# Kernel tuning notes

Measured on AMD Instinct MI355X. Metric: run time of the kernel, lower is better.

Reference implementation:

```python
import jax, jax.numpy as jnp
import numpy as np

N, E, F_IN, H, G, C = 50000, 800000, 128, 4, 32, 4
NEG_SLOPE = 0.2
EPS_GN = 1e-5


def setup_inputs() -> dict:
    key = jax.random.key(0)
    ks = iter(jax.random.split(key, 64))
    def gl(shape, fan):
        return jax.random.normal(next(ks), shape, jnp.float32) / np.float32(np.sqrt(fan))
    inp = {}
    inp['x'] = jax.random.normal(next(ks), (N, F_IN), jnp.float32)
    inp['edge_index'] = jax.random.randint(next(ks), (2, E), 0, N, dtype=jnp.int32)
    inp['batch'] = jnp.sort(jax.random.randint(next(ks), (N,), 0, G, dtype=jnp.int32))
    inp['Wl1'] = gl((F_IN, H * 64), F_IN); inp['bl1'] = jnp.zeros((H * 64,), jnp.float32)
    inp['Wr1'] = gl((F_IN, H * 64), F_IN); inp['br1'] = jnp.zeros((H * 64,), jnp.float32)
    inp['att1'] = gl((H, 64), 64); inp['bias1'] = jnp.zeros((H * 64,), jnp.float32)
    inp['gw1'] = jnp.ones((H * 64,), jnp.float32); inp['gb1'] = jnp.zeros((H * 64,), jnp.float32); inp['ga1'] = jnp.ones((H * 64,), jnp.float32)
    inp['Wl2'] = gl((256, H * 32), 256); inp['bl2'] = jnp.zeros((H * 32,), jnp.float32)
    inp['Wr2'] = gl((256, H * 32), 256); inp['br2'] = jnp.zeros((H * 32,), jnp.float32)
    inp['att2'] = gl((H, 32), 32); inp['bias2'] = jnp.zeros((H * 32,), jnp.float32)
    inp['gw2'] = jnp.ones((H * 32,), jnp.float32); inp['gb2'] = jnp.zeros((H * 32,), jnp.float32); inp['ga2'] = jnp.ones((H * 32,), jnp.float32)
    # GATv2 layer 3: 128 -> 16, 4 heads averaged (concat=False)
    inp['Wl3'] = gl((128, H * 16), 128); inp['bl3'] = jnp.zeros((H * 16,), jnp.float32)
    inp['Wr3'] = gl((128, H * 16), 128); inp['br3'] = jnp.zeros((H * 16,), jnp.float32)
    inp['att3'] = gl((H, 16), 16); inp['bias3'] = jnp.zeros((16,), jnp.float32)
    inp['gw3'] = jnp.ones((16,), jnp.float32); inp['gb3'] = jnp.zeros((16,), jnp.float32); inp['ga3'] = jnp.ones((16,), jnp.float32)
    # final linear 16 -> C
    inp['linW'] = gl((16, C), 16); inp['linB'] = jnp.zeros((C,), jnp.float32)
    return inp


def _gatv2(x, src, dst, Wl, bl, Wr, br, att, bias, D, concat):
    n = x.shape[0]
    xl = (x @ Wl + bl).reshape(n, H, D)   # source-side transform
    xr = (x @ Wr + br).reshape(n, H, D)   # target-side transform
    m = xl[src] + xr[dst]                  # [E', H, D]
    s = jnp.einsum('ehd,hd->eh', jax.nn.leaky_relu(m, NEG_SLOPE), att)
    smax = jax.ops.segment_max(s, dst, num_segments=n)
    e = jnp.exp(s - smax[dst])
    denom = jax.ops.segment_sum(e, dst, num_segments=n)
    alpha = e / (denom[dst] + 1e-16)       # softmax over incoming edges
    out = jax.ops.segment_sum(alpha[:, :, None] * xl[src], dst, num_segments=n)
    out = out.reshape(n, H * D) if concat else out.mean(axis=1)
    return out + bias


def _graphnorm(x, batch, w, b, a):
    cnt = jnp.maximum(jax.ops.segment_sum(jnp.ones((x.shape[0],), x.dtype), batch, num_segments=G), 1.0)
    mean = jax.ops.segment_sum(x, batch, num_segments=G) / cnt[:, None]
    xc = x - a * mean[batch]
    var = jax.ops.segment_sum(xc * xc, batch, num_segments=G) / cnt[:, None]
    return w * xc / jnp.sqrt(var[batch] + EPS_GN) + b


def reference(x, edge_index, batch,
              Wl1, bl1, Wr1, br1, att1, bias1, gw1, gb1, ga1,
              Wl2, bl2, Wr2, br2, att2, bias2, gw2, gb2, ga2,
              Wl3, bl3, Wr3, br3, att3, bias3, gw3, gb3, ga3,
              linW, linB):
    n = x.shape[0]
    ar = jnp.arange(n, dtype=edge_index.dtype)
    src = jnp.concatenate([edge_index[0], ar])  # add self-loops (PyG default)
    dst = jnp.concatenate([edge_index[1], ar])
    h = jax.nn.relu(_graphnorm(_gatv2(x, src, dst, Wl1, bl1, Wr1, br1, att1, bias1, 64, True), batch, gw1, gb1, ga1))
    h = jax.nn.relu(_graphnorm(_gatv2(h, src, dst, Wl2, bl2, Wr2, br2, att2, bias2, 32, True), batch, gw2, gb2, ga2))
    h = jax.nn.relu(_graphnorm(_gatv2(h, src, dst, Wl3, bl3, Wr3, br3, att3, bias3, 16, False), batch, gw3, gb3, ga3))
    cnt = jnp.maximum(jax.ops.segment_sum(jnp.ones((n,), h.dtype), batch, num_segments=G), 1.0)
    features = jax.ops.segment_sum(h, batch, num_segments=G) / cnt[:, None]  # global mean pool [G,16]
    logits = features @ linW + linB
    return (logits, features)
```

## Files before the change

kernel.cpp:

```cpp
#include <hip/hip_runtime.h>
#include <cstdint>


#define NEG_SLOPE 0.2f

typedef __attribute__((ext_vector_type(8))) short short8;
typedef __attribute__((ext_vector_type(4))) float f32x4;
typedef _Float16 h2 __attribute__((ext_vector_type(2)));
union U16 { uint4 u; short8 s; };

__device__ inline unsigned short f2bf_rne(float x) {
  unsigned u = __float_as_uint(x);
  return (unsigned short)((u + 0x7fff + ((u >> 16) & 1)) >> 16);
}
__device__ inline unsigned short f2h_bits(float x) {
  _Float16 h = (_Float16)x;
  return __builtin_bit_cast(unsigned short, h);
}
__device__ inline float h2f(unsigned short h) {
  return (float)__builtin_bit_cast(_Float16, h);
}
__device__ inline h2 u2h2(unsigned u) { return __builtin_bit_cast(h2, u); }

__device__ inline float fdot2h(h2 a, h2 b, float c) {
#if __has_builtin(__builtin_amdgcn_fdot2)
  return __builtin_amdgcn_fdot2(a, b, c, false);
#else
  return c + (float)a.x * (float)b.x + (float)a.y * (float)b.y;
#endif
}

__device__ inline int wave_incl_scan(int v, int lane) {
#pragma unroll
  for (int ofs = 1; ofs < 64; ofs <<= 1) {
    int t = __shfl_up(v, ofs, 64);
    if (lane >= ofs) v += t;
  }
  return v;
}

__global__ void deg_batch_hist(const int* __restrict__ ei, const int* __restrict__ batch,
                               int* __restrict__ deg, int* __restrict__ cnt, int E, int N) {
  __shared__ int h[32];
  if (threadIdx.x < 32) h[threadIdx.x] = 0;
  __syncthreads();
  int i = blockIdx.x * blockDim.x + threadIdx.x;
  int ET = E + N;
  if (i < ET) {
    int d = (i < E) ? ei[E + i] : (i - E);
    atomicAdd(&deg[d], 1);
  }
  if (i < N) atomicAdd(&h[batch[i]], 1);
  __syncthreads();
  if (threadIdx.x < 32 && h[threadIdx.x] > 0) atomicAdd(&cnt[threadIdx.x], h[threadIdx.x]);
}

__global__ void chunk_sums(const int* __restrict__ deg, int* __restrict__ bsum, int n) {
  int tid = threadIdx.x, lane = tid & 63, wid = tid >> 6;
  int i = blockIdx.x * 1024 + tid;
  int v = (i < n) ? deg[i] : 0;
#pragma unroll
  for (int m = 32; m; m >>= 1) v += __shfl_xor(v, m, 64);
  __shared__ int ws[16];
  if (lane == 0) ws[wid] = v;
  __syncthreads();
  if (tid == 0) {
    int s = 0;
    for (int k = 0; k < 16; ++k) s += ws[k];
    bsum[blockIdx.x] = s;
  }
}

__global__ void scan_apply(const int* __restrict__ deg, const int* __restrict__ bsum,
                           int* __restrict__ off, int nb, int n) {
  __shared__ int ws[16];
  __shared__ int sb[64];
  int tid = threadIdx.x, lane = tid & 63, wid = tid >> 6;
  if (wid == 0) {
    int v = (lane < nb) ? bsum[lane] : 0;
    int incl = wave_incl_scan(v, lane);
    sb[lane] = incl;
  }
  __syncthreads();
  int boff = (blockIdx.x > 0) ? sb[blockIdx.x - 1] : 0;
  if (blockIdx.x == 0 && tid == 0) off[n] = sb[nb - 1];
  int i = blockIdx.x * 1024 + tid;
  int v = (i < n) ? deg[i] : 0;
  int incl = wave_incl_scan(v, lane);
  if (lane == 63) ws[wid] = incl;
  __syncthreads();
  if (wid == 0) {
    int t = (lane < 16) ? ws[lane] : 0;
    t = wave_incl_scan(t, lane);
    if (lane < 16) ws[lane] = t;
  }
  __syncthreads();
  int wpre = (wid > 0) ? ws[wid - 1] : 0;
  if (i < n) off[i] = boff + wpre + incl - v;
}

__global__ void scatter_edges(const int* __restrict__ ei, const int* __restrict__ off,
                              int* __restrict__ cur, int* __restrict__ csr_src,
                              int E, int N) {
  int i = blockIdx.x * blockDim.x + threadIdx.x;
  int ET = E + N;
  if (i >= ET) return;
  int s, d;
  if (i < E) { s = ei[i]; d = ei[E + i]; } else { s = d = i - E; }
  int pos = off[d] + atomicAdd(&cur[d], 1);
  csr_src[pos] = s;
}

__device__ inline void wprep_body(const float* __restrict__ W, unsigned short* __restrict__ pk,
                                  int K, int M, int t) {
  int nk = K >> 5;
  int total = (M >> 4) * nk * 512;
  if (t >= total) return;
  int j = t & 7;
  int l = (t >> 3) & 63;
  int rest = t >> 9;
  int kc = rest % nk;
  int ct = rest / nk;
  int k = (kc << 5) + ((l >> 4) << 3) + j;
  int col = (ct << 4) + (l & 15);
  float w = W[(size_t)k * M + col];
  unsigned u = __float_as_uint(w);
  unsigned short hi = (unsigned short)(u >> 16);
  float hif = __uint_as_float(u & 0xffff0000u);
  unsigned short lo = f2bf_rne(w - hif);
  unsigned short* dst = pk + ((size_t)(ct * nk + kc) * 64 + l) * 16;
  dst[j] = hi;
  dst[j + 8] = lo;
}

__global__ void wprep_all(const float* W0, const float* W1, const float* W2,
                          const float* W3, const float* W4, const float* W5,
                          unsigned short* p0, unsigned short* p1, unsigned short* p2,
                          unsigned short* p3, unsigned short* p4, unsigned short* p5) {
  int t = blockIdx.x * 256 + threadIdx.x;
  switch (blockIdx.y) {
    case 0: wprep_body(W0, p0, 128, 256, t); break;
    case 1: wprep_body(W1, p1, 128, 256, t); break;
    case 2: wprep_body(W2, p2, 256, 128, t); break;
    case 3: wprep_body(W3, p3, 256, 128, t); break;
    case 4: wprep_body(W4, p4, 128, 64, t); break;
    default: wprep_body(W5, p5, 128, 64, t); break;
  }
}

__device__ inline void gemm_epilogue(
    unsigned short* __restrict__ sb0, unsigned short* __restrict__ sb1,
    f32x4* accL, f32x4* accR,
    const float* __restrict__ biasL, const float* __restrict__ biasR,
    unsigned short* __restrict__ CL, unsigned short* __restrict__ CR,
    int N, int M, int c0g, int row0blk) {
  int wv = threadIdx.x >> 6, lane = threadIdx.x & 63;
  int lrow0 = wv * 16 + ((lane >> 4) << 2);
  int lcolb = lane & 15;
#pragma unroll
  for (int ct = 0; ct < 4; ++ct) {
    int lcol = (ct << 4) + lcolb;
    float bvL = biasL[(c0g << 4) + lcol];
    float bvR = biasR[(c0g << 4) + lcol];
#pragma unroll
    for (int r = 0; r < 4; ++r) {
      sb0[(lrow0 + r) * 72 + lcol] = f2h_bits(accL[ct][r] + bvL);
      sb1[(lrow0 + r) * 72 + lcol] = f2h_bits(accR[ct][r] + bvR);
    }
  }
  __syncthreads();
  int tid = threadIdx.x;
#pragma unroll
  for (int pass = 0; pass < 2; ++pass) {
    int row = (tid >> 3) + (pass << 5);
    int gr = row0blk + row;
    if (gr < N) {
      int co = (tid & 7) << 3;
      uint4 vL = *(const uint4*)&sb0[row * 72 + co];
      uint4 vR = *(const uint4*)&sb1[row * 72 + co];
      size_t go = (size_t)gr * M + (c0g << 4) + co;
      *(uint4*)(CL + go) = vL;
      *(uint4*)(CR + go) = vR;
    }
  }
}

__global__ __launch_bounds__(256) void gemm_f32a_dual(
    const float* __restrict__ A,
    const uint4* __restrict__ WpkL, const uint4* __restrict__ WpkR,
    const float* __restrict__ biasL, const float* __restrict__ biasR,
    unsigned short* __restrict__ CL, unsigned short* __restrict__ CR,
    int N, int K, int M) {
  __shared__ unsigned short sb[2][64 * 72];
  int wv = threadIdx.x >> 6, lane = threadIdx.x & 63;
  int r0 = blockIdx.y * 64 + wv * 16;
  int c0g = blockIdx.x << 2;
  int row = r0 + (lane & 15);
  int kq = (lane >> 4) << 3;
  int nk = K >> 5;
  bool rok = row < N;
  const float* arow = A + (size_t)row * K;
  f32x4 accL[4], accR[4];
#pragma unroll
  for (int i = 0; i < 4; ++i) { accL[i] = (f32x4){0,0,0,0}; accR[i] = (f32x4){0,0,0,0}; }
  for (int kc = 0; kc < nk; ++kc) {
    float av[8];
    if (rok) {
      float4 t0 = *(const float4*)(arow + (kc << 5) + kq);
      float4 t1 = *(const float4*)(arow + (kc << 5) + kq + 4);
      av[0] = t0.x; av[1] = t0.y; av[2] = t0.z; av[3] = t0.w;
      av[4] = t1.x; av[5] = t1.y; av[6] = t1.z; av[7] = t1.w;
    } else {
#pragma unroll
      for (int j = 0; j < 8; ++j) av[j] = 0.f;
    }
    short8 ahi, alo;
#pragma unroll
    for (int j = 0; j < 8; ++j) {
      unsigned u = __float_as_uint(av[j]);
      ahi[j] = (short)(u >> 16);
      float hif = __uint_as_float(u & 0xffff0000u);
      alo[j] = (short)f2bf_rne(av[j] - hif);
    }
#pragma unroll
    for (int ct = 0; ct < 4; ++ct) {
      size_t fo = (((size_t)(c0g + ct) * nk + kc) * 64 + lane) * 2;
      U16 bh, bl;
      bh.u = WpkL[fo]; bl.u = WpkL[fo + 1];
      accL[ct] = __builtin_amdgcn_mfma_f32_16x16x32_bf16(alo, bh.s, accL[ct], 0, 0, 0);
      accL[ct] = __builtin_amdgcn_mfma_f32_16x16x32_bf16(ahi, bl.s, accL[ct], 0, 0, 0);
      accL[ct] = __builtin_amdgcn_mfma_f32_16x16x32_bf16(ahi, bh.s, accL[ct], 0, 0, 0);
      bh.u = WpkR[fo]; bl.u = WpkR[fo + 1];
      accR[ct] = __builtin_amdgcn_mfma_f32_16x16x32_bf16(alo, bh.s, accR[ct], 0, 0, 0);
      accR[ct] = __builtin_amdgcn_mfma_f32_16x16x32_bf16(ahi, bl.s, accR[ct], 0, 0, 0);
      accR[ct] = __builtin_amdgcn_mfma_f32_16x16x32_bf16(ahi, bh.s, accR[ct], 0, 0, 0);
    }
  }
  gemm_epilogue(sb[0], sb[1], accL, accR, biasL, biasR, CL, CR, N, M, c0g, blockIdx.y * 64);
}

__global__ __launch_bounds__(256) void gemm_bf16a_dual(
    const unsigned short* __restrict__ A,
    const uint4* __restrict__ WpkL, const uint4* __restrict__ WpkR,
    const float* __restrict__ biasL, const float* __restrict__ biasR,
    unsigned short* __restrict__ CL, unsigned short* __restrict__ CR,
    int N, int K, int M) {
  __shared__ unsigned short sb[2][64 * 72];
  int wv = threadIdx.x >> 6, lane = threadIdx.x & 63;
  int r0 = blockIdx.y * 64 + wv * 16;
  int c0g = blockIdx.x << 2;
  int row = r0 + (lane & 15);
  int kq = (lane >> 4) << 3;
  int nk = K >> 5;
  bool rok = row < N;
  const unsigned short* arow = A + (size_t)row * K;
  f32x4 accL[4], accR[4];
#pragma unroll
  for (int i = 0; i < 4; ++i) { accL[i] = (f32x4){0,0,0,0}; accR[i] = (f32x4){0,0,0,0}; }
  for (int kc = 0; kc < nk; ++kc) {
    short8 a;
    if (rok) {
      a = *(const short8*)(arow + (kc << 5) + kq);
    } else {
#pragma unroll
      for (int j = 0; j < 8; ++j) a[j] = 0;
    }
#pragma unroll
    for (int ct = 0; ct < 4; ++ct) {
      size_t fo = (((size_t)(c0g + ct) * nk + kc) * 64 + lane) * 2;
      U16 bh, bl;
      bh.u = WpkL[fo]; bl.u = WpkL[fo + 1];
      accL[ct] = __builtin_amdgcn_mfma_f32_16x16x32_bf16(a, bl.s, accL[ct], 0, 0, 0);
      accL[ct] = __builtin_amdgcn_mfma_f32_16x16x32_bf16(a, bh.s, accL[ct], 0, 0, 0);
      bh.u = WpkR[fo]; bl.u = WpkR[fo + 1];
      accR[ct] = __builtin_amdgcn_mfma_f32_16x16x32_bf16(a, bl.s, accR[ct], 0, 0, 0);
      accR[ct] = __builtin_amdgcn_mfma_f32_16x16x32_bf16(a, bh.s, accR[ct], 0, 0, 0);
    }
  }
  gemm_epilogue(sb[0], sb[1], accL, accR, biasL, biasR, CL, CR, N, M, c0g, blockIdx.y * 64);
}

template <int VEC> struct EO;

template <> struct EO<4> {
  using R = uint2;
  h2 xr0, xr1, at0, at1, sl;
  __device__ void init(const unsigned short* xrp, const float* ap) {
    uint2 rr = *(const uint2*)xrp;
    xr0 = u2h2(rr.x); xr1 = u2h2(rr.y);
    float4 a = *(const float4*)ap;
    at0 = (h2){(_Float16)a.x, (_Float16)a.y};
    at1 = (h2){(_Float16)a.z, (_Float16)a.w};
    sl = (h2){(_Float16)NEG_SLOPE, (_Float16)NEG_SLOPE};
  }
  static __device__ R ld(const unsigned short* base, size_t off) {
    return *(const uint2*)(base + off);
  }
  __device__ float score(R r) const {
    h2 t0 = u2h2(r.x) + xr0;
    h2 t1 = u2h2(r.y) + xr1;
    t0 = __builtin_elementwise_max(t0, t0 * sl);
    t1 = __builtin_elementwise_max(t1, t1 * sl);
    return fdot2h(t0, at0, fdot2h(t1, at1, 0.f));
  }
  static __device__ void accum(R r, float p, float* o) {
    h2 x0 = u2h2(r.x), x1 = u2h2(r.y);
    o[0] = fmaf(p, (float)x0.x, o[0]);
    o[1] = fmaf(p, (float)x0.y, o[1]);
    o[2] = fmaf(p, (float)x1.x, o[2]);
    o[3] = fmaf(p, (float)x1.y, o[3]);
  }
};

template <> struct EO<2> {
  using R = unsigned;
  h2 xr0, at0, sl;
  __device__ void init(const unsigned short* xrp, const float* ap) {
    xr0 = u2h2(*(const unsigned*)xrp);
    float2 a = *(const float2*)ap;
    at0 = (h2){(_Float16)a.x, (_Float16)a.y};
    sl = (h2){(_Float16)NEG_SLOPE, (_Float16)NEG_SLOPE};
  }
  static __device__ R ld(const unsigned short* base, size_t off) {
    return *(const unsigned*)(base + off);
  }
  __device__ float score(R r) const {
    h2 t0 = u2h2(r) + xr0;
    t0 = __builtin_elementwise_max(t0, t0 * sl);
    return fdot2h(t0, at0, 0.f);
  }
  static __device__ void accum(R r, float p, float* o) {
    h2 x0 = u2h2(r);
    o[0] = fmaf(p, (float)x0.x, o[0]);
    o[1] = fmaf(p, (float)x0.y, o[1]);
  }
};

template <> struct EO<1> {
  using R = unsigned short;
  float xrf, atf;
  __device__ void init(const unsigned short* xrp, const float* ap) {
    xrf = h2f(*xrp);
    atf = *ap;
  }
  static __device__ R ld(const unsigned short* base, size_t off) {
    return base[off];
  }
  __device__ float score(R r) const {
    float t = h2f(r) + xrf;
    float lk = fmaxf(t, NEG_SLOPE * t);
    return lk * atf;
  }
  static __device__ void accum(R r, float p, float* o) {
    o[0] = fmaf(p, h2f(r), o[0]);
  }
};

template <int VEC, int C>
__device__ inline void gat_chunk(const unsigned short* __restrict__ xl,
                                 const int* __restrict__ csr_src, int j, int f0,
                                 const EO<VEC>& eo, float& lrun, float* o) {
  constexpr int HD = VEC * 64;
  typename EO<VEC>::R r[C];
#pragma unroll
  for (int c = 0; c < C; ++c)
    r[c] = EO<VEC>::ld(xl, (size_t)csr_src[j + c] * HD + f0);
  float sc[C];
#pragma unroll
  for (int c = 0; c < C; ++c) sc[c] = eo.score(r[c]);
#pragma unroll
  for (int msk = 1; msk <= 8; msk <<= 1)
#pragma unroll
    for (int c = 0; c < C; ++c) sc[c] += __shfl_xor(sc[c], msk, 64);
  float p[C];
#pragma unroll
  for (int c = 0; c < C; ++c) p[c] = __expf(sc[c]);
#pragma unroll
  for (int c = 0; c < C; ++c) lrun += p[c];
#pragma unroll
  for (int c = 0; c < C; ++c) EO<VEC>::accum(r[c], p[c], o);
}

template <int VEC, bool MEANH, bool OUT16>
__global__ __launch_bounds__(256) void gat_fused(
    const unsigned short* __restrict__ xl, const unsigned short* __restrict__ xr,
    const float* __restrict__ att, const int* __restrict__ csr_src,
    const int* __restrict__ offp, const float* __restrict__ bias,
    void* __restrict__ outv, float* __restrict__ gsz, float* __restrict__ gqz,
    int n) {
  constexpr int HD = VEC * 64;
  {
    int zt = blockIdx.x * 256 + threadIdx.x;
    if (zt < 32 * 256) { gsz[zt] = 0.f; gqz[zt] = 0.f; }
  }
  int wave = (int)((blockIdx.x * (size_t)blockDim.x + threadIdx.x) >> 6);
  int lane = threadIdx.x & 63;
  if (wave >= n) return;
  const int f0 = lane * VEC;

  EO<VEC> eo;
  eo.init(xr + (size_t)wave * HD + f0, att + f0);

  float lrun = 0.f;
  float o[VEC];
#pragma unroll
  for (int v = 0; v < VEC; ++v) o[v] = 0.f;

  int beg = __builtin_amdgcn_readfirstlane(offp[wave]);
  int end = __builtin_amdgcn_readfirstlane(offp[wave + 1]);
  int j = beg;
  for (; j + 8 <= end; j += 8) gat_chunk<VEC, 8>(xl, csr_src, j, f0, eo, lrun, o);
  if (j + 4 <= end) { gat_chunk<VEC, 4>(xl, csr_src, j, f0, eo, lrun, o); j += 4; }
  for (; j < end; ++j) gat_chunk<VEC, 1>(xl, csr_src, j, f0, eo, lrun, o);

  float invl = 1.f / (lrun + 1e-16f);
  if (!MEANH) {
    if (OUT16) {
      unsigned short* out = (unsigned short*)outv;
#pragma unroll
      for (int v = 0; v < VEC; ++v)
        out[(size_t)wave * HD + f0 + v] = f2h_bits(o[v] * invl + bias[f0 + v]);
    } else {
      float* out = (float*)outv;
#pragma unroll
      for (int v = 0; v < VEC; ++v)
        out[(size_t)wave * HD + f0 + v] = o[v] * invl + bias[f0 + v];
    }
  } else {
    float val = o[0] * invl;
    val += __shfl_xor(val, 16, 64);
    val += __shfl_xor(val, 32, 64);
    val *= 0.25f;
    if (lane < 16) ((float*)outv)[(size_t)wave * 16 + lane] = val + bias[lane];
  }
}

template <int F>
__global__ void gn_stats_h(const unsigned short* __restrict__ x, const int* __restrict__ batch,
                           float* __restrict__ gsum, float* __restrict__ gsqs, int n) {
  constexpr int ROWS = 256 / F;
  int f = threadIdx.x % F;
  int r = threadIdx.x / F;
  int n0 = blockIdx.x * 128;
  float s = 0.f, q = 0.f;
  int curg = -1;
  for (int i = r; i < 128; i += ROWS) {
    int nn = n0 + i;
    if (nn >= n) break;
    int g = batch[nn];
    float v = h2f(x[(size_t)nn * F + f]);
    if (g != curg) {
      if (curg >= 0) { atomicAdd(&gsum[curg * F + f], s); atomicAdd(&gsqs[curg * F + f], q); }
      curg = g; s = 0.f; q = 0.f;
    }
    s += v; q += v * v;
  }
  if (curg >= 0) { atomicAdd(&gsum[curg * F + f], s); atomicAdd(&gsqs[curg * F + f], q); }
}

template <int F>
__global__ void gn_stats(const float* __restrict__ x, const int* __restrict__ batch,
                         float* __restrict__ gsum, float* __restrict__ gsqs, int n) {
  constexpr int ROWS = 256 / F;
  int f = threadIdx.x % F;
  int r = threadIdx.x / F;
  int n0 = blockIdx.x * 128;
  float s = 0.f, q = 0.f;
  int curg = -1;
  for (int i = r; i < 128; i += ROWS) {
    int nn = n0 + i;
    if (nn >= n) break;
    int g = batch[nn];
    float v = x[(size_t)nn * F + f];
    if (g != curg) {
      if (curg >= 0) { atomicAdd(&gsum[curg * F + f], s); atomicAdd(&gsqs[curg * F + f], q); }
      curg = g; s = 0.f; q = 0.f;
    }
    s += v; q += v * v;
  }
  if (curg >= 0) { atomicAdd(&gsum[curg * F + f], s); atomicAdd(&gsqs[curg * F + f], q); }
}

template <int F>
__global__ void gn_norm_h_bf16(const unsigned short* __restrict__ x, const int* __restrict__ batch,
                               const float* __restrict__ gsum, const float* __restrict__ gsqs,
                               const int* __restrict__ cnt,
                               const float* __restrict__ gw, const float* __restrict__ gb,
                               const float* __restrict__ ga, unsigned short* __restrict__ xo,
                               int n) {
  int idx = blockIdx.x * blockDim.x + threadIdx.x;
  if (idx >= n * F) return;
  int nn = idx / F;
  int f = idx % F;
  int g = batch[nn];
  float c = fmaxf((float)cnt[g], 1.f);
  float a = ga[f];
  float mu = gsum[g * F + f] / c;
  float var = fmaxf(gsqs[g * F + f] / c - (2.f * a - a * a) * mu * mu, 0.f);
  float rstd = rsqrtf(var + 1e-5f);
  float v = h2f(x[idx]);
  float y = gw[f] * (v - a * mu) * rstd + gb[f];
  xo[idx] = f2bf_rne(fmaxf(y, 0.f));
}

template <int F>
__global__ void gn_norm(float* __restrict__ x, const int* __restrict__ batch,
                        const float* __restrict__ gsum, const float* __restrict__ gsqs,
                        const int* __restrict__ cnt,
                        const float* __restrict__ gw, const float* __restrict__ gb,
                        const float* __restrict__ ga, int n) {
  int idx = blockIdx.x * blockDim.x + threadIdx.x;
  if (idx >= n * F) return;
  int nn = idx / F;
  int f = idx % F;
  int g = batch[nn];
  float c = fmaxf((float)cnt[g], 1.f);
  float a = ga[f];
  float mu = gsum[g * F + f] / c;
  float var = fmaxf(gsqs[g * F + f] / c - (2.f * a - a * a) * mu * mu, 0.f);
  float rstd = rsqrtf(var + 1e-5f);
  float v = x[idx];
  float y = gw[f] * (v - a * mu) * rstd + gb[f];
  x[idx] = fmaxf(y, 0.f);
}

__global__ void pool_sum(const float* __restrict__ x, const int* __restrict__ batch,
                         float* __restrict__ pooled, int n) {
  int f = threadIdx.x & 15;
  int r = threadIdx.x >> 4;
  int n0 = blockIdx.x * 128;
  float s = 0.f;
  int curg = -1;
  for (int i = r; i < 128; i += 16) {
    int nn = n0 + i;
    if (nn >= n) break;
    int g = batch[nn];
    float v = x[(size_t)nn * 16 + f];
    if (g != curg) {
      if (curg >= 0) atomicAdd(&pooled[curg * 16 + f], s);
      curg = g; s = 0.f;
    }
    s += v;
  }
  if (curg >= 0) atomicAdd(&pooled[curg * 16 + f], s);
}

__global__ void finalize(const float* __restrict__ pooled, const int* __restrict__ cnt,
                         const float* __restrict__ linW, const float* __restrict__ linB,
                         float* __restrict__ out) {
  __shared__ float feat[32 * 16];
  int tid = threadIdx.x;
  {
    int g = tid >> 4;
    float c = fmaxf((float)cnt[g], 1.f);
    float v = pooled[tid] / c;
    feat[tid] = v;
    out[128 + tid] = v;
  }
  __syncthreads();
  if (tid < 128) {
    int g = tid >> 2, c = tid & 3;
    float s = linB[c];
#pragma unroll
    for (int k = 0; k < 16; ++k) s += feat[g * 16 + k] * linW[k * 4 + c];
    out[g * 4 + c] = s;
  }
}

extern "C" void kernel_launch(void* const* d_in, const int* in_sizes, int n_in,
                              void* d_out, int out_size, void* d_ws, size_t ws_size,
                              hipStream_t stream) {
  const float* x     = (const float*)d_in[0];
  const int*   ei    = (const int*)d_in[1];
  const int*   batch = (const int*)d_in[2];
  const float* Wl1 = (const float*)d_in[3];
  const float* bl1 = (const float*)d_in[4];
  const float* Wr1 = (const float*)d_in[5];
  const float* br1 = (const float*)d_in[6];
  const float* att1 = (const float*)d_in[7];
  const float* bias1 = (const float*)d_in[8];
  const float* gw1 = (const float*)d_in[9];
  const float* gb1 = (const float*)d_in[10];
  const float* ga1 = (const float*)d_in[11];
  const float* Wl2 = (const float*)d_in[12];
  const float* bl2 = (const float*)d_in[13];
  const float* Wr2 = (const float*)d_in[14];
  const float* br2 = (const float*)d_in[15];
  const float* att2 = (const float*)d_in[16];
  const float* bias2 = (const float*)d_in[17];
  const float* gw2 = (const float*)d_in[18];
  const float* gb2 = (const float*)d_in[19];
  const float* ga2 = (const float*)d_in[20];
  const float* Wl3 = (const float*)d_in[21];
  const float* bl3 = (const float*)d_in[22];
  const float* Wr3 = (const float*)d_in[23];
  const float* br3 = (const float*)d_in[24];
  const float* att3 = (const float*)d_in[25];
  const float* bias3 = (const float*)d_in[26];
  const float* gw3 = (const float*)d_in[27];
  const float* gb3 = (const float*)d_in[28];
  const float* ga3 = (const float*)d_in[29];
  const float* linW = (const float*)d_in[30];
  const float* linB = (const float*)d_in[31];
  float* out = (float*)d_out;

  const int N  = in_sizes[2];
  const int E  = in_sizes[1] / 2;
  const int ET = E + N;

  char* w = (char*)d_ws;
  float* P = (float*)w;             w += (size_t)N * 256 * 4;
  unsigned short* Ph = (unsigned short*)P;
  unsigned short* Pb = (unsigned short*)w; w += (size_t)N * 256 * 2;
  unsigned short* Qb = (unsigned short*)w; w += (size_t)N * 256 * 2;
  unsigned short* Rb = (unsigned short*)w; w += (size_t)N * 256 * 2;
  int* csr_src = (int*)w;           w += (size_t)ET * 4;
  int* offp = (int*)w;              w += (size_t)(N + 1) * 4;
  int* bsum = (int*)w;              w += 64 * 4;
  char* z0 = w;
  int* deg  = (int*)w;              w += (size_t)N * 4;
  int* cur  = (int*)w;              w += (size_t)N * 4;
  int* cnt  = (int*)w;              w += 32 * 4;
  float* pooled = (float*)w;        w += 512 * 4;
  float* gsum  = (float*)w;         w += 32 * 256 * 4;
  float* gsqs  = (float*)w;         w += 32 * 256 * 4;
  size_t zbytes = (size_t)(w - z0);
  uintptr_t wal = ((uintptr_t)w + 15) & ~(uintptr_t)15;
  uint4* wpk1l = (uint4*)wal;
  uint4* wpk1r = wpk1l + 8192;
  uint4* wpk2l = wpk1r + 8192;
  uint4* wpk2r = wpk2l + 8192;
  uint4* wpk3l = wpk2r + 8192;
  uint4* wpk3r = wpk3l + 2048;

  (void)hipMemsetAsync(z0, 0, zbytes, stream);

  wprep_all<<<dim3(128, 6), 256, 0, stream>>>(
      Wl1, Wr1, Wl2, Wr2, Wl3, Wr3,
      (unsigned short*)wpk1l, (unsigned short*)wpk1r,
      (unsigned short*)wpk2l, (unsigned short*)wpk2r,
      (unsigned short*)wpk3l, (unsigned short*)wpk3r);

  int nb = (N + 1023) / 1024;
  deg_batch_hist<<<(ET + 255) / 256, 256, 0, stream>>>(ei, batch, deg, cnt, E, N);
  chunk_sums<<<nb, 1024, 0, stream>>>(deg, bsum, N);
  scan_apply<<<nb, 1024, 0, stream>>>(deg, bsum, offp, nb, N);
  scatter_edges<<<(ET + 255) / 256, 256, 0, stream>>>(ei, offp, cur, csr_src, E, N);

  int gry = (N + 63) / 64;
  {
    gemm_f32a_dual<<<dim3(4, gry), 256, 0, stream>>>(x, wpk1l, wpk1r, bl1, br1, Qb, Rb, N, 128, 256);
    gat_fused<4, false, true><<<(N + 3) / 4, 256, 0, stream>>>(Qb, Rb, att1, csr_src, offp, bias1, Ph, gsum, gsqs, N);
    gn_stats_h<256><<<(N + 127) / 128, 256, 0, stream>>>(Ph, batch, gsum, gsqs, N);
    gn_norm_h_bf16<256><<<(int)(((size_t)N * 256 + 255) / 256), 256, 0, stream>>>(Ph, batch, gsum, gsqs, cnt, gw1, gb1, ga1, Pb, N);
  }
  {
    gemm_bf16a_dual<<<dim3(2, gry), 256, 0, stream>>>(Pb, wpk2l, wpk2r, bl2, br2, Qb, Rb, N, 256, 128);
    gat_fused<2, false, true><<<(N + 3) / 4, 256, 0, stream>>>(Qb, Rb, att2, csr_src, offp, bias2, Ph, gsum, gsqs, N);
    gn_stats_h<128><<<(N + 127) / 128, 256, 0, stream>>>(Ph, batch, gsum, gsqs, N);
    gn_norm_h_bf16<128><<<(int)(((size_t)N * 128 + 255) / 256), 256, 0, stream>>>(Ph, batch, gsum, gsqs, cnt, gw2, gb2, ga2, Pb, N);
  }
  {
    gemm_bf16a_dual<<<dim3(1, gry), 256, 0, stream>>>(Pb, wpk3l, wpk3r, bl3, br3, Qb, Rb, N, 128, 64);
    gat_fused<1, true, false><<<(N + 3) / 4, 256, 0, stream>>>(Qb, Rb, att3, csr_src, offp, bias3, P, gsum, gsqs, N);
    gn_stats<16><<<(N + 127) / 128, 256, 0, stream>>>(P, batch, gsum, gsqs, N);
    gn_norm<16><<<(int)(((size_t)N * 16 + 255) / 256), 256, 0, stream>>>(P, batch, gsum, gsqs, cnt, gw3, gb3, ga3, N);
  }
  pool_sum<<<(N + 127) / 128, 256, 0, stream>>>(P, batch, pooled, N);
  finalize<<<1, 512, 0, stream>>>(pooled, cnt, linW, linB, out);
}
```

Measured before the change: 646.9 us.

## Fuse GraphNorm normalize and ReLU into next GEMM load and pooling

Replaces the separate per-element GraphNorm normalize kernels with a tiny kernel that builds per-group scale and shift tables. The scale, shift, ReLU and bf16 conversion are then applied while the next layer's GEMM loads its A operand, and inside the final pooling kernel. This removes the full-size normalized intermediate buffers and their extra read and write passes, at the cost of extra table loads and ALU work in the GEMM inner loop. Gather offsets in the attention kernel also switch from size_t to 32-bit unsigned arithmetic.

```diff
diff --git a/kernel.cpp b/kernel.cpp
--- a/kernel.cpp
+++ b/kernel.cpp
@@ -239,8 +239,9 @@
   gemm_epilogue(sb[0], sb[1], accL, accR, biasL, biasR, CL, CR, N, M, c0g, blockIdx.y * 64);
 }
 
-__global__ __launch_bounds__(256) void gemm_bf16a_dual(
-    const unsigned short* __restrict__ A,
+__global__ __launch_bounds__(256) void gemm_norm_dual(
+    const unsigned short* __restrict__ A, const int* __restrict__ batch,
+    const float* __restrict__ sc, const float* __restrict__ sh,
     const uint4* __restrict__ WpkL, const uint4* __restrict__ WpkR,
     const float* __restrict__ biasL, const float* __restrict__ biasR,
     unsigned short* __restrict__ CL, unsigned short* __restrict__ CR,
@@ -254,13 +255,32 @@
   int nk = K >> 5;
   bool rok = row < N;
   const unsigned short* arow = A + (size_t)row * K;
+  int gF = rok ? batch[row] * K : 0;
   f32x4 accL[4], accR[4];
 #pragma unroll
   for (int i = 0; i < 4; ++i) { accL[i] = (f32x4){0,0,0,0}; accR[i] = (f32x4){0,0,0,0}; }
   for (int kc = 0; kc < nk; ++kc) {
     short8 a;
     if (rok) {
-      a = *(const short8*)(arow + (kc << 5) + kq);
+      int kf = (kc << 5) + kq;
+      uint4 araw = *(const uint4*)(arow + kf);
+      float4 s0 = *(const float4*)(sc + gF + kf);
+      float4 s1 = *(const float4*)(sc + gF + kf + 4);
+      float4 h0 = *(const float4*)(sh + gF + kf);
+      float4 h1 = *(const float4*)(sh + gF + kf + 4);
+      h2 p0 = u2h2(araw.x), p1 = u2h2(araw.y), p2 = u2h2(araw.z), p3 = u2h2(araw.w);
+      float y0 = fmaxf(fmaf((float)p0.x, s0.x, h0.x), 0.f);
+      float y1 = fmaxf(fmaf((float)p0.y, s0.y, h0.y), 0.f);
+      float y2 = fmaxf(fmaf((float)p1.x, s0.z, h0.z), 0.f);
+      float y3 = fmaxf(fmaf((float)p1.y, s0.w, h0.w), 0.f);
+      float y4 = fmaxf(fmaf((float)p2.x, s1.x, h1.x), 0.f);
+      float y5 = fmaxf(fmaf((float)p2.y, s1.y, h1.y), 0.f);
+      float y6 = fmaxf(fmaf((float)p3.x, s1.z, h1.z), 0.f);
+      float y7 = fmaxf(fmaf((float)p3.y, s1.w, h1.w), 0.f);
+      a[0] = (short)f2bf_rne(y0); a[1] = (short)f2bf_rne(y1);
+      a[2] = (short)f2bf_rne(y2); a[3] = (short)f2bf_rne(y3);
+      a[4] = (short)f2bf_rne(y4); a[5] = (short)f2bf_rne(y5);
+      a[6] = (short)f2bf_rne(y6); a[7] = (short)f2bf_rne(y7);
     } else {
 #pragma unroll
       for (int j = 0; j < 8; ++j) a[j] = 0;
@@ -293,7 +313,7 @@
     at1 = (h2){(_Float16)a.z, (_Float16)a.w};
     sl = (h2){(_Float16)NEG_SLOPE, (_Float16)NEG_SLOPE};
   }
-  static __device__ R ld(const unsigned short* base, size_t off) {
+  static __device__ R ld(const unsigned short* base, unsigned off) {
     return *(const uint2*)(base + off);
   }
   __device__ float score(R r) const {
@@ -321,7 +341,7 @@
     at0 = (h2){(_Float16)a.x, (_Float16)a.y};
     sl = (h2){(_Float16)NEG_SLOPE, (_Float16)NEG_SLOPE};
   }
-  static __device__ R ld(const unsigned short* base, size_t off) {
+  static __device__ R ld(const unsigned short* base, unsigned off) {
     return *(const unsigned*)(base + off);
   }
   __device__ float score(R r) const {
@@ -343,7 +363,7 @@
     xrf = h2f(*xrp);
     atf = *ap;
   }
-  static __device__ R ld(const unsigned short* base, size_t off) {
+  static __device__ R ld(const unsigned short* base, unsigned off) {
     return base[off];
   }
   __device__ float score(R r) const {
@@ -364,7 +384,7 @@
   typename EO<VEC>::R r[C];
 #pragma unroll
   for (int c = 0; c < C; ++c)
-    r[c] = EO<VEC>::ld(xl, (size_t)csr_src[j + c] * HD + f0);
+    r[c] = EO<VEC>::ld(xl, (unsigned)csr_src[j + c] * HD + f0);
   float sc[C];
 #pragma unroll
   for (int c = 0; c < C; ++c) sc[c] = eo.score(r[c]);
@@ -481,66 +501,44 @@
   if (curg >= 0) { atomicAdd(&gsum[curg * F + f], s); atomicAdd(&gsqs[curg * F + f], q); }
 }
 
-template <int F>
-__global__ void gn_norm_h_bf16(const unsigned short* __restrict__ x, const int* __restrict__ batch,
-                               const float* __restrict__ gsum, const float* __restrict__ gsqs,
-                               const int* __restrict__ cnt,
-                               const float* __restrict__ gw, const float* __restrict__ gb,
-                               const float* __restrict__ ga, unsigned short* __restrict__ xo,
-                               int n) {
+__global__ void gn_final(const float* __restrict__ gsum, const float* __restrict__ gsqs,
+                         const int* __restrict__ cnt, const float* __restrict__ gw,
+                         const float* __restrict__ gb, const float* __restrict__ ga,
+                         float* __restrict__ sc, float* __restrict__ sh, int F) {
   int idx = blockIdx.x * blockDim.x + threadIdx.x;
-  if (idx >= n * F) return;
-  int nn = idx / F;
-  int f = idx % F;
-  int g = batch[nn];
+  if (idx >= 32 * F) return;
+  int g = idx / F, f = idx - g * F;
   float c = fmaxf((float)cnt[g], 1.f);
   float a = ga[f];
-  float mu = gsum[g * F + f] / c;
-  float var = fmaxf(gsqs[g * F + f] / c - (2.f * a - a * a) * mu * mu, 0.f);
+  float mu = gsum[idx] / c;
+  float var = fmaxf(gsqs[idx] / c - (2.f * a - a * a) * mu * mu, 0.f);
   float rstd = rsqrtf(var + 1e-5f);
-  float v = h2f(x[idx]);
-  float y = gw[f] * (v - a * mu) * rstd + gb[f];
-  xo[idx] = f2bf_rne(fmaxf(y, 0.f));
-}
-
-template <int F>
-__global__ void gn_norm(float* __restrict__ x, const int* __restrict__ batch,
-                        const float* __restrict__ gsum, const float* __restrict__ gsqs,
-                        const int* __restrict__ cnt,
-                        const float* __restrict__ gw, const float* __restrict__ gb,
-                        const float* __restrict__ ga, int n) {
-  int idx = blockIdx.x * blockDim.x + threadIdx.x;
-  if (idx >= n * F) return;
-  int nn = idx / F;
-  int f = idx % F;
-  int g = batch[nn];
-  float c = fmaxf((float)cnt[g], 1.f);
-  float a = ga[f];
-  float mu = gsum[g * F + f] / c;
-  float var = fmaxf(gsqs[g * F + f] / c - (2.f * a - a * a) * mu * mu, 0.f);
-  float rstd = rsqrtf(var + 1e-5f);
-  float v = x[idx];
-  float y = gw[f] * (v - a * mu) * rstd + gb[f];
-  x[idx] = fmaxf(y, 0.f);
-}
-
-__global__ void pool_sum(const float* __restrict__ x, const int* __restrict__ batch,
-                         float* __restrict__ pooled, int n) {
+  float w = gw[f] * rstd;
+  sc[idx] = w;
+  sh[idx] = gb[f] - w * a * mu;
+}
+
+__global__ void norm_pool(const float* __restrict__ x, const int* __restrict__ batch,
+                          const float* __restrict__ sc, const float* __restrict__ sh,
+                          float* __restrict__ pooled, int n) {
   int f = threadIdx.x & 15;
   int r = threadIdx.x >> 4;
   int n0 = blockIdx.x * 128;
   float s = 0.f;
   int curg = -1;
+  float scv = 0.f, shv = 0.f;
   for (int i = r; i < 128; i += 16) {
     int nn = n0 + i;
     if (nn >= n) break;
     int g = batch[nn];
-    float v = x[(size_t)nn * 16 + f];
     if (g != curg) {
       if (curg >= 0) atomicAdd(&pooled[curg * 16 + f], s);
       curg = g; s = 0.f;
-    }
-    s += v;
+      scv = sc[g * 16 + f];
+      shv = sh[g * 16 + f];
+    }
+    float v = x[(size_t)nn * 16 + f];
+    s += fmaxf(fmaf(v, scv, shv), 0.f);
   }
   if (curg >= 0) atomicAdd(&pooled[curg * 16 + f], s);
 }
@@ -611,12 +609,13 @@
   char* w = (char*)d_ws;
   float* P = (float*)w;             w += (size_t)N * 256 * 4;
   unsigned short* Ph = (unsigned short*)P;
-  unsigned short* Pb = (unsigned short*)w; w += (size_t)N * 256 * 2;
   unsigned short* Qb = (unsigned short*)w; w += (size_t)N * 256 * 2;
   unsigned short* Rb = (unsigned short*)w; w += (size_t)N * 256 * 2;
   int* csr_src = (int*)w;           w += (size_t)ET * 4;
   int* offp = (int*)w;              w += (size_t)(N + 1) * 4;
   int* bsum = (int*)w;              w += 64 * 4;
+  float* scb = (float*)w;           w += 32 * 256 * 4;
+  float* shb = (float*)w;           w += 32 * 256 * 4;
   char* z0 = w;
   int* deg  = (int*)w;              w += (size_t)N * 4;
   int* cur  = (int*)w;              w += (size_t)N * 4;
@@ -648,24 +647,18 @@
   scatter_edges<<<(ET + 255) / 256, 256, 0, stream>>>(ei, offp, cur, csr_src, E, N);
 
   int gry = (N + 63) / 64;
-  {
-    gemm_f32a_dual<<<dim3(4, gry), 256, 0, stream>>>(x, wpk1l, wpk1r, bl1, br1, Qb, Rb, N, 128, 256);
-    gat_fused<4, false, true><<<(N + 3) / 4, 256, 0, stream>>>(Qb, Rb, att1, csr_src, offp, bias1, Ph, gsum, gsqs, N);
-    gn_stats_h<256><<<(N + 127) / 128, 256, 0, stream>>>(Ph, batch, gsum, gsqs, N);
-    gn_norm_h_bf16<256><<<(int)(((size_t)N * 256 + 255) / 256), 256, 0, stream>>>(Ph, batch, gsum, gsqs, cnt, gw1, gb1, ga1, Pb, N);
-  }
-  {
-    gemm_bf16a_dual<<<dim3(2, gry), 256, 0, stream>>>(Pb, wpk2l, wpk2r, bl2, br2, Qb, Rb, N, 256, 128);
-    gat_fused<2, false, true><<<(N + 3) / 4, 256, 0, stream>>>(Qb, Rb, att2, csr_src, offp, bias2, Ph, gsum, gsqs, N);
-    gn_stats_h<128><<<(N + 127) / 128, 256, 0, stream>>>(Ph, batch, gsum, gsqs, N);
-    gn_norm_h_bf16<128><<<(int)(((size_t)N * 128 + 255) / 256), 256, 0, stream>>>(Ph, batch, gsum, gsqs, cnt, gw2, gb2, ga2, Pb, N);
-  }
-  {
-    gemm_bf16a_dual<<<dim3(1, gry), 256, 0, stream>>>(Pb, wpk3l, wpk3r, bl3, br3, Qb, Rb, N, 128, 64);
-    gat_fused<1, true, false><<<(N + 3) / 4, 256, 0, stream>>>(Qb, Rb, att3, csr_src, offp, bias3, P, gsum, gsqs, N);
-    gn_stats<16><<<(N + 127) / 128, 256, 0, stream>>>(P, batch, gsum, gsqs, N);
-    gn_norm<16><<<(int)(((size_t)N * 16 + 255) / 256), 256, 0, stream>>>(P, batch, gsum, gsqs, cnt, gw3, gb3, ga3, N);
-  }
-  pool_sum<<<(N + 127) / 128, 256, 0, stream>>>(P, batch, pooled, N);
+  gemm_f32a_dual<<<dim3(4, gry), 256, 0, stream>>>(x, wpk1l, wpk1r, bl1, br1, Qb, Rb, N, 128, 256);
+  gat_fused<4, false, true><<<(N + 3) / 4, 256, 0, stream>>>(Qb, Rb, att1, csr_src, offp, bias1, Ph, gsum, gsqs, N);
+  gn_stats_h<256><<<(N + 127) / 128, 256, 0, stream>>>(Ph, batch, gsum, gsqs, N);
+  gn_final<<<32, 256, 0, stream>>>(gsum, gsqs, cnt, gw1, gb1, ga1, scb, shb, 256);
+  gemm_norm_dual<<<dim3(2, gry), 256, 0, stream>>>(Ph, batch, scb, shb, wpk2l, wpk2r, bl2, br2, Qb, Rb, N, 256, 128);
+  gat_fused<2, false, true><<<(N + 3) / 4, 256, 0, stream>>>(Qb, Rb, att2, csr_src, offp, bias2, Ph, gsum, gsqs, N);
+  gn_stats_h<128><<<(N + 127) / 128, 256, 0, stream>>>(Ph, batch, gsum, gsqs, N);
+  gn_final<<<16, 256, 0, stream>>>(gsum, gsqs, cnt, gw2, gb2, ga2, scb, shb, 128);
+  gemm_norm_dual<<<dim3(1, gry), 256, 0, stream>>>(Ph, batch, scb, shb, wpk3l, wpk3r, bl3, br3, Qb, Rb, N, 128, 64);
+  gat_fused<1, true, false><<<(N + 3) / 4, 256, 0, stream>>>(Qb, Rb, att3, csr_src, offp, bias3, P, gsum, gsqs, N);
+  gn_stats<16><<<(N + 127) / 128, 256, 0, stream>>>(P, batch, gsum, gsqs, N);
+  gn_final<<<2, 256, 0, stream>>>(gsum, gsqs, cnt, gw3, gb3, ga3, scb, shb, 16);
+  norm_pool<<<(N + 127) / 128, 256, 0, stream>>>(P, batch, scb, shb, pooled, N);
   finalize<<<1, 512, 0, stream>>>(pooled, cnt, linW, linB, out);
 }
```

New measurement: 612.3 us. 1.06x faster.
